# Performance work log

Measured on AMD Instinct MI355X. Metric: run time of the kernel, lower is better.

The kernel has to match this reference:

```python
import jax, jax.numpy as jnp
import numpy as np

NUM_CLASSES = 1000
N_CENTER = 3
B = 524288
D = 64  # fixed by nn.Linear(64, 1)


def setup_inputs() -> dict:
    key = jax.random.key(0)
    k1, k2, k3, k4, k5 = jax.random.split(key, 5)
    x = jax.random.normal(k1, (B, D), dtype=jnp.float32)
    labels = jax.random.randint(k2, (B,), 0, NUM_CLASSES, dtype=jnp.int64)
    lin_w = jax.random.normal(k3, (1, D), dtype=jnp.float32) * (1.0 / np.sqrt(D))
    lin_b = jnp.zeros((1,), dtype=jnp.float32)
    linear_p = jax.random.normal(k4, (NUM_CLASSES, 1, N_CENTER), dtype=jnp.float32)
    bias_p = jnp.ones((NUM_CLASSES, N_CENTER), dtype=jnp.float32)
    centers = jnp.zeros((NUM_CLASSES, N_CENTER, 1), dtype=jnp.float32) + 0.01 * jax.random.normal(k5, (NUM_CLASSES, N_CENTER, 1), dtype=jnp.float32)
    return {"x": x, "labels": labels, "lin_w": lin_w, "lin_b": lin_b,
            "linear_p": linear_p, "bias_p": bias_p, "centers": centers}


def reference(x, labels, lin_w, lin_b, linear_p, bias_p, centers):
    # maps_detach = x.detach(); maps_detach_p = lin(maps_detach) -> [B, 1]
    xd = jax.lax.stop_gradient(x)
    maps_p = xd @ lin_w.T + lin_b  # [B, 1]

    # gather per-label params
    lin_sel = linear_p[labels, 0, :]   # [B, n_center]
    b_sel = bias_p[labels]             # [B, n_center]
    c_sel = centers[labels, :, 0]      # [B, n_center]

    # bmm([B,1,1],[B,1,n]) + bias -> logits [B, n]; softmax over centers
    logits = maps_p * lin_sel + b_sel
    gamma = jax.nn.softmax(logits, axis=1)  # [B, n_center]

    # sum_d (x[b,d] - c[b,n])^2 = ||x||^2 - 2 c * sum(x) + D * c^2  (avoids [B,n,D])
    xsq = jnp.sum(x * x, axis=1, keepdims=True)   # [B, 1]
    xs = jnp.sum(x, axis=1, keepdims=True)        # [B, 1]
    d = jnp.float32(x.shape[1])
    sqdist = xsq - 2.0 * c_sel * xs + d * c_sel * c_sel  # [B, n_center]

    loss = jnp.sum(gamma * sqdist) / x.shape[0]
    return loss
```

## Files before the change

### kernel.cpp

```cpp
#include <hip/hip_runtime.h>

#define B_ROWS 524288
#define D_DIM 64

__global__ __launch_bounds__(256) void mcl_kernel(
    const float* __restrict__ x,
    const int* __restrict__ labels,
    const float* __restrict__ lin_w,
    const float* __restrict__ lin_b,
    const float* __restrict__ linear_p,
    const float* __restrict__ bias_p,
    const float* __restrict__ centers,
    float* __restrict__ out)
{
    const int tid        = blockIdx.x * blockDim.x + threadIdx.x;
    const int lane       = threadIdx.x & 63;
    const int sub        = lane & 3;
    const int rowInWave  = lane >> 2;
    const int waveGlobal = tid >> 6;
    const int totalWaves = (gridDim.x * blockDim.x) >> 6;
    const int rowsPerIter = totalWaves * 16;

    const float4 lw0 = ((const float4*)lin_w)[sub + 0];
    const float4 lw1 = ((const float4*)lin_w)[sub + 4];
    const float4 lw2 = ((const float4*)lin_w)[sub + 8];
    const float4 lw3 = ((const float4*)lin_w)[sub + 12];
    const float  lb  = lin_b[0];

    float acc = 0.0f;

    for (int row = waveGlobal * 16 + rowInWave; row < B_ROWS; row += rowsPerIter) {
        const float4* xr = (const float4*)(x + (size_t)row * D_DIM);
        const float4 x0 = xr[sub + 0];
        const float4 x1 = xr[sub + 4];
        const float4 x2 = xr[sub + 8];
        const float4 x3 = xr[sub + 12];

        float sd = x0.x*lw0.x + x0.y*lw0.y + x0.z*lw0.z + x0.w*lw0.w
                 + x1.x*lw1.x + x1.y*lw1.y + x1.z*lw1.z + x1.w*lw1.w
                 + x2.x*lw2.x + x2.y*lw2.y + x2.z*lw2.z + x2.w*lw2.w
                 + x3.x*lw3.x + x3.y*lw3.y + x3.z*lw3.z + x3.w*lw3.w;
        float ss = (x0.x + x0.y + x0.z + x0.w) + (x1.x + x1.y + x1.z + x1.w)
                 + (x2.x + x2.y + x2.z + x2.w) + (x3.x + x3.y + x3.z + x3.w);
        float sq = x0.x*x0.x + x0.y*x0.y + x0.z*x0.z + x0.w*x0.w
                 + x1.x*x1.x + x1.y*x1.y + x1.z*x1.z + x1.w*x1.w
                 + x2.x*x2.x + x2.y*x2.y + x2.z*x2.z + x2.w*x2.w
                 + x3.x*x3.x + x3.y*x3.y + x3.z*x3.z + x3.w*x3.w;

        #pragma unroll
        for (int off = 1; off < 4; off <<= 1) {
            sd += __shfl_xor(sd, off, 64);
            ss += __shfl_xor(ss, off, 64);
            sq += __shfl_xor(sq, off, 64);
        }

        const int lab = labels[row];
        const float maps = sd + lb;

        const float p0 = linear_p[lab * 3 + 0];
        const float p1 = linear_p[lab * 3 + 1];
        const float p2 = linear_p[lab * 3 + 2];
        const float b0 = bias_p[lab * 3 + 0];
        const float b1 = bias_p[lab * 3 + 1];
        const float b2 = bias_p[lab * 3 + 2];
        const float c0 = centers[lab * 3 + 0];
        const float c1 = centers[lab * 3 + 1];
        const float c2 = centers[lab * 3 + 2];

        const float l0 = maps * p0 + b0;
        const float l1 = maps * p1 + b1;
        const float l2 = maps * p2 + b2;

        const float m  = fmaxf(l0, fmaxf(l1, l2));
        const float e0 = __expf(l0 - m);
        const float e1 = __expf(l1 - m);
        const float e2 = __expf(l2 - m);
        const float denom = e0 + e1 + e2;

        const float dD = (float)D_DIM;
        const float s0 = sq - 2.0f * c0 * ss + dD * c0 * c0;
        const float s1 = sq - 2.0f * c1 * ss + dD * c1 * c1;
        const float s2 = sq - 2.0f * c2 * ss + dD * c2 * c2;

        acc += (e0 * s0 + e1 * s1 + e2 * s2) / denom;
    }

    #pragma unroll
    for (int off = 1; off < 64; off <<= 1)
        acc += __shfl_xor(acc, off, 64);

    __shared__ float waveSums[4];
    if (lane == 0) waveSums[threadIdx.x >> 6] = acc;
    __syncthreads();
    if (threadIdx.x == 0) {
        float s = waveSums[0] + waveSums[1] + waveSums[2] + waveSums[3];
        atomicAdd(out, s * (0.25f / (float)B_ROWS));
    }
}

extern "C" void kernel_launch(void* const* d_in, const int* in_sizes, int n_in,
                              void* d_out, int out_size, void* d_ws, size_t ws_size,
                              hipStream_t stream) {
    const float* x        = (const float*)d_in[0];
    const int*   labels   = (const int*)d_in[1];
    const float* lin_w    = (const float*)d_in[2];
    const float* lin_b    = (const float*)d_in[3];
    const float* linear_p = (const float*)d_in[4];
    const float* bias_p   = (const float*)d_in[5];
    const float* centers  = (const float*)d_in[6];
    float* out = (float*)d_out;

    hipMemsetAsync(out, 0, sizeof(float), stream);

    dim3 grid(2048), block(256);
    mcl_kernel<<<grid, block, 0, stream>>>(x, labels, lin_w, lin_b,
                                           linear_p, bias_p, centers, out);
}
```

Before: 208.4 us.

## Replace memset and atomics with two-pass reduction, fully unroll fixed row loop

Drops the hipMemsetAsync and per-block atomicAdd. Each block now writes a partial sum to workspace, and a single-block finalize kernel reduces the 2048 partials. The main row loop gets a compile-time trip count and is fully unrolled, which lets loads from several iterations be issued early. The division is replaced by a hardware reciprocal. The cost is a second kernel launch, more register pressure from unrolling, and a small loss of precision in the reciprocal.

```diff
diff --git a/kernel.cpp b/kernel.cpp
--- a/kernel.cpp
+++ b/kernel.cpp
@@ -2,8 +2,12 @@
 
 #define B_ROWS 524288
 #define D_DIM 64
+#define GRID 2048
+#define BLOCK 256
+#define ROWS_PER_ITER ((GRID * BLOCK / 64) * 16)
+#define N_ITERS (B_ROWS / ROWS_PER_ITER)
 
-__global__ __launch_bounds__(256) void mcl_kernel(
+__global__ __launch_bounds__(BLOCK) void mcl_main(
     const float* __restrict__ x,
     const int* __restrict__ labels,
     const float* __restrict__ lin_w,
@@ -11,15 +15,13 @@
     const float* __restrict__ linear_p,
     const float* __restrict__ bias_p,
     const float* __restrict__ centers,
-    float* __restrict__ out)
+    float* __restrict__ partials)
 {
-    const int tid        = blockIdx.x * blockDim.x + threadIdx.x;
+    const int tid        = blockIdx.x * BLOCK + threadIdx.x;
     const int lane       = threadIdx.x & 63;
     const int sub        = lane & 3;
     const int rowInWave  = lane >> 2;
     const int waveGlobal = tid >> 6;
-    const int totalWaves = (gridDim.x * blockDim.x) >> 6;
-    const int rowsPerIter = totalWaves * 16;
 
     const float4 lw0 = ((const float4*)lin_w)[sub + 0];
     const float4 lw1 = ((const float4*)lin_w)[sub + 4];
@@ -28,8 +30,10 @@
     const float  lb  = lin_b[0];
 
     float acc = 0.0f;
+    int row = waveGlobal * 16 + rowInWave;
 
-    for (int row = waveGlobal * 16 + rowInWave; row < B_ROWS; row += rowsPerIter) {
+    #pragma unroll
+    for (int it = 0; it < N_ITERS; ++it, row += ROWS_PER_ITER) {
         const float4* xr = (const float4*)(x + (size_t)row * D_DIM);
         const float4 x0 = xr[sub + 0];
         const float4 x1 = xr[sub + 4];
@@ -75,26 +79,48 @@
         const float e0 = __expf(l0 - m);
         const float e1 = __expf(l1 - m);
         const float e2 = __expf(l2 - m);
-        const float denom = e0 + e1 + e2;
+        const float rdenom = __builtin_amdgcn_rcpf(e0 + e1 + e2);
 
         const float dD = (float)D_DIM;
         const float s0 = sq - 2.0f * c0 * ss + dD * c0 * c0;
         const float s1 = sq - 2.0f * c1 * ss + dD * c1 * c1;
         const float s2 = sq - 2.0f * c2 * ss + dD * c2 * c2;
 
-        acc += (e0 * s0 + e1 * s1 + e2 * s2) / denom;
+        acc += (e0 * s0 + e1 * s1 + e2 * s2) * rdenom;
     }
 
     #pragma unroll
     for (int off = 1; off < 64; off <<= 1)
         acc += __shfl_xor(acc, off, 64);
 
-    __shared__ float waveSums[4];
+    __shared__ float waveSums[BLOCK / 64];
     if (lane == 0) waveSums[threadIdx.x >> 6] = acc;
     __syncthreads();
     if (threadIdx.x == 0) {
         float s = waveSums[0] + waveSums[1] + waveSums[2] + waveSums[3];
-        atomicAdd(out, s * (0.25f / (float)B_ROWS));
+        partials[blockIdx.x] = s;
+    }
+}
+
+__global__ __launch_bounds__(BLOCK) void mcl_finalize(
+    const float* __restrict__ partials, float* __restrict__ out)
+{
+    float acc = 0.0f;
+    #pragma unroll
+    for (int i = threadIdx.x; i < GRID; i += BLOCK)
+        acc += partials[i];
+
+    const int lane = threadIdx.x & 63;
+    #pragma unroll
+    for (int off = 1; off < 64; off <<= 1)
+        acc += __shfl_xor(acc, off, 64);
+
+    __shared__ float waveSums[BLOCK / 64];
+    if (lane == 0) waveSums[threadIdx.x >> 6] = acc;
+    __syncthreads();
+    if (threadIdx.x == 0) {
+        float s = waveSums[0] + waveSums[1] + waveSums[2] + waveSums[3];
+        out[0] = s * (0.25f / (float)B_ROWS);
     }
 }
 
@@ -108,11 +134,10 @@
     const float* linear_p = (const float*)d_in[4];
     const float* bias_p   = (const float*)d_in[5];
     const float* centers  = (const float*)d_in[6];
-    float* out = (float*)d_out;
+    float* out      = (float*)d_out;
+    float* partials = (float*)d_ws;
 
-    hipMemsetAsync(out, 0, sizeof(float), stream);
-
-    dim3 grid(2048), block(256);
-    mcl_kernel<<<grid, block, 0, stream>>>(x, labels, lin_w, lin_b,
-                                           linear_p, bias_p, centers, out);
+    mcl_main<<<dim3(GRID), dim3(BLOCK), 0, stream>>>(
+        x, labels, lin_w, lin_b, linear_p, bias_p, centers, partials);
+    mcl_finalize<<<dim3(1), dim3(BLOCK), 0, stream>>>(partials, out);
 }
```

Measured after the change: 198.4 us. -4.8%, faster.
